# Optimization experiments

Measured on AMD Instinct MI355X. Metric: run time of the kernel, lower is better.

Reference implementation:

```python
import jax, jax.numpy as jnp
import numpy as np

B, TQ, TP, D = 4, 512, 512, 256


def setup_inputs() -> dict:
    key = jax.random.key(0)
    ks = jax.random.split(key, 5)
    return {
        "q": jax.random.normal(ks[0], (B, TQ, D), dtype=jnp.float32),
        "p": jax.random.normal(ks[1], (B, TP, D), dtype=jnp.float32),
        "W0": jax.random.normal(ks[2], (D, D), dtype=jnp.float32) / np.sqrt(D),
        "W1": jax.random.normal(ks[3], (D, D), dtype=jnp.float32) / np.sqrt(D),
        "vc": jax.random.normal(ks[4], (D, 1), dtype=jnp.float32) * 0.05,
    }


def reference(q, p, W0, W1, vc):
    # q: [B,Tq,Dq], p: [B,Tp,Dp]
    prod_q = jnp.einsum('bqd,de->bqe', q, W0)   # [B,Tq,dim]
    prod_p = jnp.einsum('bpd,de->bpe', p, W1)   # [B,Tp,dim]
    # additive attention energies: tanh over broadcast sum [B,Tp,Tq,dim]
    energy = jnp.tanh(prod_p[:, :, None, :] + prod_q[:, None, :, :])
    scores = jnp.einsum('bpqe,e->bpq', energy, vc[:, 0])  # [B,Tp,Tq]
    # original softmax is over axis=-2 of [B,Tp,Tq], i.e. the Tp axis
    weights = jax.nn.softmax(scores, axis=1)   # [B,Tp,Tq]
    # weighted sum over the Tq axis of (tiled) q
    attention_q = jnp.einsum('bpq,bqd->bpd', weights, q)  # [B,Tp,Dq]
    return attention_q
```

## Files before the change

kernel.cpp:

```cpp
#include <hip/hip_runtime.h>

#define NB 4
#define TT 512
#define DD 256
#define K2L2E    2.885390081777927f
#define NEG2L2E (-2.885390081777927f)

#if defined(__has_builtin)
# if __has_builtin(__builtin_amdgcn_global_load_lds)
#  define HAS_GLL 1
# endif
#endif

typedef float v2f __attribute__((ext_vector_type(2)));

__device__ __forceinline__ v2f pk_fma(v2f a, v2f b, v2f c) {
#if defined(__has_builtin)
# if __has_builtin(__builtin_elementwise_fma)
    return __builtin_elementwise_fma(a, b, c);
# else
    v2f r; r.x = __builtin_fmaf(a.x, b.x, c.x); r.y = __builtin_fmaf(a.y, b.y, c.y); return r;
# endif
#else
    v2f r; r.x = __builtin_fmaf(a.x, b.x, c.x); r.y = __builtin_fmaf(a.y, b.y, c.y); return r;
#endif
}
__device__ __forceinline__ v2f splat2(float s) { v2f r; r.x = s; r.y = s; return r; }

__device__ __forceinline__ void stage16(const float* __restrict__ g, float* l) {
#ifdef HAS_GLL
    __builtin_amdgcn_global_load_lds((const __attribute__((address_space(1))) void*)g,
                                     (__attribute__((address_space(3))) void*)l, 16, 0, 0);
#else
    *(float4*)l = *(const float4*)g;
#endif
}

__global__ __launch_bounds__(256) void proj_exp_kernel(
    const float* __restrict__ qin, const float* __restrict__ pin,
    const float* __restrict__ W0, const float* __restrict__ W1,
    float* __restrict__ expQ, float* __restrict__ expP)
{
    const int blk = blockIdx.x;
    const int wh = blk >> 8, tid = blk & 255;
    const int m0 = (tid >> 2) * 32, n0 = (tid & 3) * 64;
    const float* A = wh ? pin : qin;
    const float* W = wh ? W1 : W0;

    __shared__ __align__(16) float As[32 * 34];
    __shared__ __align__(16) float Bs[32 * 64];

    const int t  = threadIdx.x;
    const int ar = t >> 3, ac4 = (t & 7) * 4;
    const int br = t >> 4, bc4 = (t & 15) * 4;
    const int tm = wh ? (t >> 4) : (t & 15);
    const int tn = wh ? (t & 15) : (t >> 4);

    const float* Ap = A + (long)(m0 + ar) * DD + ac4;

    float4 av  = *(const float4*)Ap;
    float4 bv0 = *(const float4*)(W + (long)br * DD + n0 + bc4);
    float4 bv1 = *(const float4*)(W + (long)(br + 16) * DD + n0 + bc4);

    v2f accv[2][2];
    accv[0][0] = splat2(0.f); accv[0][1] = splat2(0.f);
    accv[1][0] = splat2(0.f); accv[1][1] = splat2(0.f);

    for (int c = 0; c < 8; ++c) {
        As[(ac4 + 0) * 34 + ar] = av.x;
        As[(ac4 + 1) * 34 + ar] = av.y;
        As[(ac4 + 2) * 34 + ar] = av.z;
        As[(ac4 + 3) * 34 + ar] = av.w;
        *(float4*)&Bs[br * 64 + bc4]        = bv0;
        *(float4*)&Bs[(br + 16) * 64 + bc4] = bv1;
        __syncthreads();
        if (c < 7) {
            int k1 = (c + 1) * 32;
            av  = *(const float4*)(Ap + k1);
            bv0 = *(const float4*)(W + (long)(k1 + br) * DD + n0 + bc4);
            bv1 = *(const float4*)(W + (long)(k1 + 16 + br) * DD + n0 + bc4);
        }
        #pragma unroll
        for (int kk = 0; kk < 32; ++kk) {
            float2 a = *(const float2*)&As[kk * 34 + 2 * tm];
            float4 b = *(const float4*)&Bs[kk * 64 + 4 * tn];
            v2f b01; b01.x = b.x; b01.y = b.y;
            v2f b23; b23.x = b.z; b23.y = b.w;
            accv[0][0] = pk_fma(splat2(a.x), b01, accv[0][0]);
            accv[0][1] = pk_fma(splat2(a.x), b23, accv[0][1]);
            accv[1][0] = pk_fma(splat2(a.y), b01, accv[1][0]);
            accv[1][1] = pk_fma(splat2(a.y), b23, accv[1][1]);
        }
        __syncthreads();
    }

    float acc[2][4];
    #pragma unroll
    for (int i = 0; i < 2; ++i) {
        acc[i][0] = accv[i][0].x; acc[i][1] = accv[i][0].y;
        acc[i][2] = accv[i][1].x; acc[i][3] = accv[i][1].y;
    }

    const int bi = m0 >> 9;
    const int ml = m0 & 511;
    if (wh) {
        #pragma unroll
        for (int i = 0; i < 2; ++i) {
            float4 st;
            st.x = __builtin_amdgcn_exp2f(acc[i][0] * K2L2E);
            st.y = __builtin_amdgcn_exp2f(acc[i][1] * K2L2E);
            st.z = __builtin_amdgcn_exp2f(acc[i][2] * K2L2E);
            st.w = __builtin_amdgcn_exp2f(acc[i][3] * K2L2E);
            *(float4*)(expP + ((long)bi * TT + ml + 2 * tm + i) * DD + n0 + 4 * tn) = st;
        }
    } else {
        #pragma unroll
        for (int j = 0; j < 4; ++j) {
            int d = n0 + 4 * tn + j;
            float2 st;
            st.x = __builtin_amdgcn_exp2f(acc[0][j] * K2L2E);
            st.y = __builtin_amdgcn_exp2f(acc[1][j] * K2L2E);
            *(float2*)(expQ + ((long)bi * DD + d) * TT + ml + 2 * tm) = st;
        }
    }
}

__global__ __launch_bounds__(512, 6) void score_kernel(
    const float* __restrict__ expP, const float* __restrict__ expQ,
    const float* __restrict__ vc, float* __restrict__ ebuf, float* __restrict__ lpart)
{
    const int b = blockIdx.z, pt = blockIdx.y, qt = blockIdx.x;
    const int p0 = pt * 32, q0 = qt * 64;
    const int t  = threadIdx.x;
    const int qx = t & 31, py = t >> 5;

    __shared__ __align__(16) float PA[32 * 128];
    __shared__ __align__(16) float QB[128 * 64];
    __shared__ __align__(16) float vcs[DD];

    const float* gP = expP + ((long)b * TT + p0) * DD;
    const float* gQ = expQ + (long)b * DD * TT + q0;

    #pragma unroll
    for (int s = 0; s < 2; ++s) {
        int f = t + 512 * s, pr = f >> 5, d4 = (f & 31) * 4;
        stage16(gP + (long)pr * DD + d4, &PA[f * 4]);
    }
    #pragma unroll
    for (int s = 0; s < 4; ++s) {
        int f = t + 512 * s, d = f >> 4, o4 = (f & 15) * 4;
        stage16(gQ + (long)d * TT + o4, &QB[f * 4]);
    }
    if (t < DD) vcs[t] = vc[t];
    __syncthreads();

    v2f acc[2]; acc[0] = splat2(0.f); acc[1] = splat2(0.f);
    const v2f one = splat2(1.0f);

    for (int c = 0; c < 2; ++c) {
        if (c == 1) {
            __syncthreads();
            #pragma unroll
            for (int s = 0; s < 2; ++s) {
                int f = t + 512 * s, pr = f >> 5, d4 = (f & 31) * 4;
                stage16(gP + (long)pr * DD + 128 + d4, &PA[f * 4]);
            }
            #pragma unroll
            for (int s = 0; s < 4; ++s) {
                int f = t + 512 * s, d = f >> 4, o4 = (f & 15) * 4;
                stage16(gQ + (long)(128 + d) * TT + o4, &QB[f * 4]);
            }
            __syncthreads();
        }
        const float* vcb = &vcs[c * 128];
        #pragma unroll 4
        for (int dq = 0; dq < 32; ++dq) {
            float4 vq = *(const float4*)&vcb[4 * dq];
            float4 aq0 = *(const float4*)&PA[(2 * py) * 128 + 4 * dq];
            float4 aq1 = *(const float4*)&PA[(2 * py + 1) * 128 + 4 * dq];
            v2f B0 = *(const v2f*)&QB[(4 * dq + 0) * 64 + 2 * qx];
            v2f B1 = *(const v2f*)&QB[(4 * dq + 1) * 64 + 2 * qx];
            v2f B2 = *(const v2f*)&QB[(4 * dq + 2) * 64 + 2 * qx];
            v2f B3 = *(const v2f*)&QB[(4 * dq + 3) * 64 + 2 * qx];
            #pragma unroll
            for (int i = 0; i < 2; ++i) {
                float4 a = i ? aq1 : aq0;
                v2f f0 = pk_fma(splat2(a.x), B0, one);
                v2f f1 = pk_fma(splat2(a.y), B1, one);
                v2f f2 = pk_fma(splat2(a.z), B2, one);
                v2f f3 = pk_fma(splat2(a.w), B3, one);
                v2f t01 = f0 * f1;
                v2f t23 = f2 * f3;
                v2f den = t01 * t23;
                v2f n01 = pk_fma(splat2(vq.x), f1, splat2(vq.y) * f0);
                v2f n23 = pk_fma(splat2(vq.z), f3, splat2(vq.w) * f2);
                v2f num = pk_fma(n01, t23, n23 * t01);
                v2f r;
                r.x = __builtin_amdgcn_rcpf(den.x);
                r.y = __builtin_amdgcn_rcpf(den.y);
                acc[i] = pk_fma(num, r, acc[i]);
            }
        }
    }

    float* eb = ebuf + ((long)b * TT + p0) * TT + q0;
    v2f colp = splat2(0.f);
    #pragma unroll
    for (int i = 0; i < 2; ++i) {
        float2 ev;
        ev.x = __builtin_amdgcn_exp2f(acc[i].x * NEG2L2E);
        ev.y = __builtin_amdgcn_exp2f(acc[i].y * NEG2L2E);
        *(float2*)(eb + (long)(2 * py + i) * TT + 2 * qx) = ev;
        colp.x += ev.x; colp.y += ev.y;
    }
    __syncthreads();
    float* scr = (float*)&PA[0];
    *(float2*)&scr[py * 64 + 2 * qx] = make_float2(colp.x, colp.y);
    __syncthreads();
    if (t < 64) {
        float s = 0.f;
        #pragma unroll
        for (int r = 0; r < 16; ++r) s += scr[r * 64 + t];
        lpart[((long)b * 16 + pt) * TT + q0 + t] = s;
    }
}

__global__ __launch_bounds__(256) void out_kernel(
    const float* __restrict__ ebuf, const float* __restrict__ qin,
    const float* __restrict__ lpart, float* __restrict__ out)
{
    const int b = blockIdx.z, pt = blockIdx.y, dt = blockIdx.x;
    const int m0 = pt * 32, n0 = dt * 32;
    const int t    = threadIdx.x;
    const int wv   = t >> 6;
    const int lane = t & 63;
    const int pg   = lane >> 3;
    const int dg   = lane & 7;

    __shared__ __align__(16) float smem[4 * 32 * 36];
    __shared__ float linv[TT];
    float* As = smem;
    float* Bs = smem + 64 * 36;

    #pragma unroll
    for (int s = 0; s < 2; ++s) {
        int qq = t + 256 * s;
        float sum = 0.f;
        #pragma unroll
        for (int pb = 0; pb < 16; ++pb) sum += lpart[((long)b * 16 + pb) * TT + qq];
        linv[qq] = __builtin_amdgcn_rcpf(sum);
    }
    __syncthreads();

    const float* Ab = ebuf + ((long)b * TT + m0) * TT;
    const float* Bb = qin + (long)b * TT * DD + n0;

    const int ar = t >> 3, ak4 = (t & 7) * 4;

    v2f acc[4][2];
    #pragma unroll
    for (int i = 0; i < 4; ++i) { acc[i][0] = splat2(0.f); acc[i][1] = splat2(0.f); }

    for (int c = 0; c < 8; ++c) {
        const int k0 = c * 64;
        #pragma unroll
        for (int s = 0; s < 2; ++s) {
            int f = t + 256 * s, kr = f >> 3, d4 = (f & 7) * 4;
            stage16(Bb + (long)(k0 + kr) * DD + d4, &Bs[f * 4]);
        }
        #pragma unroll
        for (int s = 0; s < 2; ++s) {
            int kq = ak4 + 32 * s;
            float4 a = *(const float4*)(Ab + (long)ar * TT + k0 + kq);
            float4 lv = *(const float4*)&linv[k0 + kq];
            As[(kq + 0) * 36 + ar] = a.x * lv.x;
            As[(kq + 1) * 36 + ar] = a.y * lv.y;
            As[(kq + 2) * 36 + ar] = a.z * lv.z;
            As[(kq + 3) * 36 + ar] = a.w * lv.w;
        }
        __syncthreads();
        const int kb = 16 * wv;
        #pragma unroll
        for (int u = 0; u < 16; ++u) {
            int kk = kb + u;
            float4 a  = *(const float4*)&As[kk * 36 + 4 * pg];
            float4 bq = *(const float4*)&Bs[kk * 32 + 4 * dg];
            v2f b0; b0.x = bq.x; b0.y = bq.y;
            v2f b1; b1.x = bq.z; b1.y = bq.w;
            acc[0][0] = pk_fma(splat2(a.x), b0, acc[0][0]);
            acc[0][1] = pk_fma(splat2(a.x), b1, acc[0][1]);
            acc[1][0] = pk_fma(splat2(a.y), b0, acc[1][0]);
            acc[1][1] = pk_fma(splat2(a.y), b1, acc[1][1]);
            acc[2][0] = pk_fma(splat2(a.z), b0, acc[2][0]);
            acc[2][1] = pk_fma(splat2(a.z), b1, acc[2][1]);
            acc[3][0] = pk_fma(splat2(a.w), b0, acc[3][0]);
            acc[3][1] = pk_fma(splat2(a.w), b1, acc[3][1]);
        }
        __syncthreads();
    }

    float* scr = smem;
    #pragma unroll
    for (int i = 0; i < 4; ++i) {
        *(v2f*)&scr[wv * 1152 + (4 * pg + i) * 36 + 4 * dg]     = acc[i][0];
        *(v2f*)&scr[wv * 1152 + (4 * pg + i) * 36 + 4 * dg + 2] = acc[i][1];
    }
    __syncthreads();
    {
        int pr = t >> 3, d0 = (t & 7) * 4;
        float4 s0 = *(const float4*)&scr[0 * 1152 + pr * 36 + d0];
        float4 s1 = *(const float4*)&scr[1 * 1152 + pr * 36 + d0];
        float4 s2 = *(const float4*)&scr[2 * 1152 + pr * 36 + d0];
        float4 s3 = *(const float4*)&scr[3 * 1152 + pr * 36 + d0];
        float4 v;
        v.x = (s0.x + s1.x) + (s2.x + s3.x);
        v.y = (s0.y + s1.y) + (s2.y + s3.y);
        v.z = (s0.z + s1.z) + (s2.z + s3.z);
        v.w = (s0.w + s1.w) + (s2.w + s3.w);
        *(float4*)(out + ((long)b * TT + m0 + pr) * DD + n0 + d0) = v;
    }
}

extern "C" void kernel_launch(void* const* d_in, const int* in_sizes, int n_in,
                              void* d_out, int out_size, void* d_ws, size_t ws_size,
                              hipStream_t stream) {
    const float* q  = (const float*)d_in[0];
    const float* p  = (const float*)d_in[1];
    const float* W0 = (const float*)d_in[2];
    const float* W1 = (const float*)d_in[3];
    const float* vc = (const float*)d_in[4];
    float* out = (float*)d_out;

    float* ws    = (float*)d_ws;
    float* expQ  = ws;
    float* expP  = ws + 524288;
    float* ebuf  = ws + 1048576;
    float* lpart = ws + 2097152;

    proj_exp_kernel<<<dim3(512), 256, 0, stream>>>(q, p, W0, W1, expQ, expP);
    score_kernel<<<dim3(8, 16, NB), 512, 0, stream>>>(expP, expQ, vc, ebuf, lpart);
    out_kernel<<<dim3(8, 16, NB), 256, 0, stream>>>(ebuf, q, lpart, out);
}
```

Baseline: 118.6 us.

## Enlarge score tile to 64x64 per block with double-buffered LDS staging

The score kernel now has each block cover 64 p rows by 64 q columns with 256 threads, and each thread computes a 4x4 register tile instead of 2x2. The D dimension is streamed in four 64-wide chunks through double-buffered LDS, with an XOR swizzle on P rows to avoid bank conflicts. This raises arithmetic reuse per LDS load and overlaps the global-to-LDS copy with compute. In exchange the grid is halved to 256 blocks, which may reduce occupancy on a large GPU, and register pressure grows.

```diff
diff --git a/kernel.cpp b/kernel.cpp
--- a/kernel.cpp
+++ b/kernel.cpp
@@ -125,103 +125,138 @@
     }
 }
 
-__global__ __launch_bounds__(512, 6) void score_kernel(
+__global__ __launch_bounds__(256) void score_kernel(
     const float* __restrict__ expP, const float* __restrict__ expQ,
     const float* __restrict__ vc, float* __restrict__ ebuf, float* __restrict__ lpart)
 {
     const int b = blockIdx.z, pt = blockIdx.y, qt = blockIdx.x;
-    const int p0 = pt * 32, q0 = qt * 64;
+    const int p0 = pt * 64, q0 = qt * 64;
     const int t  = threadIdx.x;
-    const int qx = t & 31, py = t >> 5;
-
-    __shared__ __align__(16) float PA[32 * 128];
-    __shared__ __align__(16) float QB[128 * 64];
+    const int qx = t & 15;
+    const int py = t >> 4;
+    const int sw = py & 3;
+
+    __shared__ __align__(16) float PA[2][64 * 64];
+    __shared__ __align__(16) float QB[2][64 * 64];
     __shared__ __align__(16) float vcs[DD];
 
     const float* gP = expP + ((long)b * TT + p0) * DD;
     const float* gQ = expQ + (long)b * DD * TT + q0;
 
     #pragma unroll
-    for (int s = 0; s < 2; ++s) {
-        int f = t + 512 * s, pr = f >> 5, d4 = (f & 31) * 4;
-        stage16(gP + (long)pr * DD + d4, &PA[f * 4]);
-    }
-    #pragma unroll
     for (int s = 0; s < 4; ++s) {
-        int f = t + 512 * s, d = f >> 4, o4 = (f & 15) * 4;
-        stage16(gQ + (long)d * TT + o4, &QB[f * 4]);
-    }
-    if (t < DD) vcs[t] = vc[t];
+        int f = t + 256 * s, pr = f >> 4, j = f & 15;
+        stage16(gP + (long)pr * DD + 4 * (j ^ ((pr >> 2) & 3)), &PA[0][f * 4]);
+    }
+    #pragma unroll
+    for (int s = 0; s < 4; ++s) {
+        int f = t + 256 * s, d = f >> 4, o4 = (f & 15) * 4;
+        stage16(gQ + (long)d * TT + o4, &QB[0][f * 4]);
+    }
+    vcs[t] = vc[t];
     __syncthreads();
 
-    v2f acc[2]; acc[0] = splat2(0.f); acc[1] = splat2(0.f);
+    v2f acc[4][2];
+    #pragma unroll
+    for (int i = 0; i < 4; ++i) { acc[i][0] = splat2(0.f); acc[i][1] = splat2(0.f); }
     const v2f one = splat2(1.0f);
 
-    for (int c = 0; c < 2; ++c) {
-        if (c == 1) {
-            __syncthreads();
+    int buf = 0;
+    for (int c = 0; c < 4; ++c) {
+        if (c < 3) {
+            const float* gPc = gP + (c + 1) * 64;
+            const float* gQc = gQ + (long)(c + 1) * 64 * TT;
             #pragma unroll
-            for (int s = 0; s < 2; ++s) {
-                int f = t + 512 * s, pr = f >> 5, d4 = (f & 31) * 4;
-                stage16(gP + (long)pr * DD + 128 + d4, &PA[f * 4]);
+            for (int s = 0; s < 4; ++s) {
+                int f = t + 256 * s, pr = f >> 4, j = f & 15;
+                stage16(gPc + (long)pr * DD + 4 * (j ^ ((pr >> 2) & 3)), &PA[buf ^ 1][f * 4]);
             }
             #pragma unroll
             for (int s = 0; s < 4; ++s) {
-                int f = t + 512 * s, d = f >> 4, o4 = (f & 15) * 4;
-                stage16(gQ + (long)(128 + d) * TT + o4, &QB[f * 4]);
+                int f = t + 256 * s, d = f >> 4, o4 = (f & 15) * 4;
+                stage16(gQc + (long)d * TT + o4, &QB[buf ^ 1][f * 4]);
             }
-            __syncthreads();
-        }
-        const float* vcb = &vcs[c * 128];
+        }
+        const float* vcb = &vcs[c * 64];
+        const float* pa = &PA[buf][0];
+        const float* qb = &QB[buf][0];
         #pragma unroll 4
-        for (int dq = 0; dq < 32; ++dq) {
+        for (int dq = 0; dq < 16; ++dq) {
             float4 vq = *(const float4*)&vcb[4 * dq];
-            float4 aq0 = *(const float4*)&PA[(2 * py) * 128 + 4 * dq];
-            float4 aq1 = *(const float4*)&PA[(2 * py + 1) * 128 + 4 * dq];
-            v2f B0 = *(const v2f*)&QB[(4 * dq + 0) * 64 + 2 * qx];
-            v2f B1 = *(const v2f*)&QB[(4 * dq + 1) * 64 + 2 * qx];
-            v2f B2 = *(const v2f*)&QB[(4 * dq + 2) * 64 + 2 * qx];
-            v2f B3 = *(const v2f*)&QB[(4 * dq + 3) * 64 + 2 * qx];
+            float4 B0 = *(const float4*)&qb[(4 * dq + 0) * 64 + 4 * qx];
+            float4 B1 = *(const float4*)&qb[(4 * dq + 1) * 64 + 4 * qx];
+            float4 B2 = *(const float4*)&qb[(4 * dq + 2) * 64 + 4 * qx];
+            float4 B3 = *(const float4*)&qb[(4 * dq + 3) * 64 + 4 * qx];
+            const int sq = 4 * (dq ^ sw);
+            float4 A0 = *(const float4*)&pa[(4 * py + 0) * 64 + sq];
+            float4 A1 = *(const float4*)&pa[(4 * py + 1) * 64 + sq];
+            float4 A2 = *(const float4*)&pa[(4 * py + 2) * 64 + sq];
+            float4 A3 = *(const float4*)&pa[(4 * py + 3) * 64 + sq];
+            v2f b0l; b0l.x = B0.x; b0l.y = B0.y;  v2f b0h; b0h.x = B0.z; b0h.y = B0.w;
+            v2f b1l; b1l.x = B1.x; b1l.y = B1.y;  v2f b1h; b1h.x = B1.z; b1h.y = B1.w;
+            v2f b2l; b2l.x = B2.x; b2l.y = B2.y;  v2f b2h; b2h.x = B2.z; b2h.y = B2.w;
+            v2f b3l; b3l.x = B3.x; b3l.y = B3.y;  v2f b3h; b3h.x = B3.z; b3h.y = B3.w;
             #pragma unroll
-            for (int i = 0; i < 2; ++i) {
-                float4 a = i ? aq1 : aq0;
-                v2f f0 = pk_fma(splat2(a.x), B0, one);
-                v2f f1 = pk_fma(splat2(a.y), B1, one);
-                v2f f2 = pk_fma(splat2(a.z), B2, one);
-                v2f f3 = pk_fma(splat2(a.w), B3, one);
-                v2f t01 = f0 * f1;
-                v2f t23 = f2 * f3;
-                v2f den = t01 * t23;
-                v2f n01 = pk_fma(splat2(vq.x), f1, splat2(vq.y) * f0);
-                v2f n23 = pk_fma(splat2(vq.z), f3, splat2(vq.w) * f2);
-                v2f num = pk_fma(n01, t23, n23 * t01);
-                v2f r;
-                r.x = __builtin_amdgcn_rcpf(den.x);
-                r.y = __builtin_amdgcn_rcpf(den.y);
-                acc[i] = pk_fma(num, r, acc[i]);
+            for (int i = 0; i < 4; ++i) {
+                float4 a = (i == 0) ? A0 : (i == 1) ? A1 : (i == 2) ? A2 : A3;
+                {
+                    v2f f0 = pk_fma(splat2(a.x), b0l, one);
+                    v2f f1 = pk_fma(splat2(a.y), b1l, one);
+                    v2f f2 = pk_fma(splat2(a.z), b2l, one);
+                    v2f f3 = pk_fma(splat2(a.w), b3l, one);
+                    v2f t01 = f0 * f1;
+                    v2f t23 = f2 * f3;
+                    v2f den = t01 * t23;
+                    v2f n01 = pk_fma(splat2(vq.x), f1, splat2(vq.y) * f0);
+                    v2f n23 = pk_fma(splat2(vq.z), f3, splat2(vq.w) * f2);
+                    v2f num = pk_fma(n01, t23, n23 * t01);
+                    v2f r;
+                    r.x = __builtin_amdgcn_rcpf(den.x);
+                    r.y = __builtin_amdgcn_rcpf(den.y);
+                    acc[i][0] = pk_fma(num, r, acc[i][0]);
+                }
+                {
+                    v2f f0 = pk_fma(splat2(a.x), b0h, one);
+                    v2f f1 = pk_fma(splat2(a.y), b1h, one);
+                    v2f f2 = pk_fma(splat2(a.z), b2h, one);
+                    v2f f3 = pk_fma(splat2(a.w), b3h, one);
+                    v2f t01 = f0 * f1;
+                    v2f t23 = f2 * f3;
+                    v2f den = t01 * t23;
+                    v2f n01 = pk_fma(splat2(vq.x), f1, splat2(vq.y) * f0);
+                    v2f n23 = pk_fma(splat2(vq.z), f3, splat2(vq.w) * f2);
+                    v2f num = pk_fma(n01, t23, n23 * t01);
+                    v2f r;
+                    r.x = __builtin_amdgcn_rcpf(den.x);
+                    r.y = __builtin_amdgcn_rcpf(den.y);
+                    acc[i][1] = pk_fma(num, r, acc[i][1]);
+                }
             }
         }
+        __syncthreads();
+        buf ^= 1;
     }
 
     float* eb = ebuf + ((long)b * TT + p0) * TT + q0;
-    v2f colp = splat2(0.f);
-    #pragma unroll
-    for (int i = 0; i < 2; ++i) {
-        float2 ev;
-        ev.x = __builtin_amdgcn_exp2f(acc[i].x * NEG2L2E);
-        ev.y = __builtin_amdgcn_exp2f(acc[i].y * NEG2L2E);
-        *(float2*)(eb + (long)(2 * py + i) * TT + 2 * qx) = ev;
-        colp.x += ev.x; colp.y += ev.y;
-    }
-    __syncthreads();
-    float* scr = (float*)&PA[0];
-    *(float2*)&scr[py * 64 + 2 * qx] = make_float2(colp.x, colp.y);
+    float4 colp; colp.x = 0.f; colp.y = 0.f; colp.z = 0.f; colp.w = 0.f;
+    #pragma unroll
+    for (int i = 0; i < 4; ++i) {
+        float4 ev;
+        ev.x = __builtin_amdgcn_exp2f(acc[i][0].x * NEG2L2E);
+        ev.y = __builtin_amdgcn_exp2f(acc[i][0].y * NEG2L2E);
+        ev.z = __builtin_amdgcn_exp2f(acc[i][1].x * NEG2L2E);
+        ev.w = __builtin_amdgcn_exp2f(acc[i][1].y * NEG2L2E);
+        *(float4*)(eb + (long)(4 * py + i) * TT + 4 * qx) = ev;
+        colp.x += ev.x; colp.y += ev.y; colp.z += ev.z; colp.w += ev.w;
+    }
+    float* scr = &PA[0][0];
+    *(float4*)&scr[py * 64 + 4 * qx] = colp;
     __syncthreads();
     if (t < 64) {
         float s = 0.f;
         #pragma unroll
         for (int r = 0; r < 16; ++r) s += scr[r * 64 + t];
-        lpart[((long)b * 16 + pt) * TT + q0 + t] = s;
+        lpart[((long)b * 8 + pt) * TT + q0 + t] = s;
     }
 }
 
@@ -247,7 +282,7 @@
         int qq = t + 256 * s;
         float sum = 0.f;
         #pragma unroll
-        for (int pb = 0; pb < 16; ++pb) sum += lpart[((long)b * 16 + pb) * TT + qq];
+        for (int pb = 0; pb < 8; ++pb) sum += lpart[((long)b * 8 + pb) * TT + qq];
         linv[qq] = __builtin_amdgcn_rcpf(sum);
     }
     __syncthreads();
@@ -338,6 +373,6 @@
     float* lpart = ws + 2097152;
 
     proj_exp_kernel<<<dim3(512), 256, 0, stream>>>(q, p, W0, W1, expQ, expP);
-    score_kernel<<<dim3(8, 16, NB), 512, 0, stream>>>(expP, expQ, vc, ebuf, lpart);
+    score_kernel<<<dim3(8, 8, NB), 256, 0, stream>>>(expP, expQ, vc, ebuf, lpart);
     out_kernel<<<dim3(8, 16, NB), 256, 0, stream>>>(ebuf, q, lpart, out);
 }
```

After: 120.9 us. About the same (+1.9%).
